# Performance work log

Measured on AMD Instinct MI355X. Metric: run time of the kernel, lower is better.

## Reference

```python
import jax, jax.numpy as jnp
import numpy as np

COUNTS = [1536, 8192, 16384, 24576, 12288, 1024, 512, 512, 256, 128, 128]
OFFS = np.concatenate([[0], np.cumsum(COUNTS)]).astype(int).tolist()
N = OFFS[-1]          # 65536 atoms total, sorted by degree
MAX_DEG = 10
BATCH = 2048          # fixed GraphGather batch size
F_IN = 75
GC = 256
DENSE = 512
N_TASKS = 12
N_CLASSES = 2
BN_EPS = 1e-3         # keras BatchNormalization default epsilon


def _graph_conv(x, deg_adjs, w0, wself, wneigh, b):
    # deepchem GraphConv: per-degree (self @ Wself + sum_neighbors @ Wneigh + b), relu
    outs = [x[OFFS[0]:OFFS[1]] @ w0 + b[0]]  # degree-0 atoms: self transform only
    for d in range(1, MAX_DEG + 1):
        self_atoms = x[OFFS[d]:OFFS[d + 1]]            # [n_d, F]
        neigh = x[deg_adjs[d - 1]].sum(axis=1)         # gather [n_d, d, F] -> sum -> [n_d, F]
        outs.append(self_atoms @ wself[d - 1] + neigh @ wneigh[d - 1] + b[d])
    return jax.nn.relu(jnp.concatenate(outs, axis=0))


def _graph_pool(x, deg_adjs):
    # deepchem GraphPool: elementwise max over {self} U neighbors, per degree
    outs = [x[OFFS[0]:OFFS[1]]]  # degree-0 atoms pass through
    for d in range(1, MAX_DEG + 1):
        self_atoms = x[OFFS[d]:OFFS[d + 1]]
        outs.append(jnp.maximum(self_atoms, x[deg_adjs[d - 1]].max(axis=1)))
    return jnp.concatenate(outs, axis=0)


def _bn(x, g, bta, m, v):
    # inference-mode BatchNormalization (training=False -> moving stats)
    return g * (x - m) * jax.lax.rsqrt(v + BN_EPS) + bta


def setup_inputs():
    key = jax.random.key(0)
    ks = iter(jax.random.split(key, 64))
    inp = {}
    inp["atom_features"] = jax.random.normal(next(ks), (N, F_IN), jnp.float32)
    inp["degree_slice"] = jnp.asarray(
        np.stack([np.array(OFFS[:-1]), np.array(COUNTS)], axis=1), jnp.int32)
    # each molecule gets exactly N/BATCH atoms so no GraphGather segment is empty
    inp["membership"] = jax.random.permutation(
        next(ks), jnp.arange(N, dtype=jnp.int32) % BATCH)
    inp["n_samples"] = BATCH
    for d in range(1, MAX_DEG + 1):
        inp["deg_adj_%d" % d] = jax.random.randint(
            next(ks), (COUNTS[d], d), 0, N, jnp.int32)

    def lin(k, fi, fo):
        return jax.random.normal(k, (fi, fo), jnp.float32) * np.float32(1.0 / np.sqrt(fi))

    for li, fi in [(1, F_IN), (2, GC)]:
        inp["gc%d_w0" % li] = lin(next(ks), fi, GC)
        inp["gc%d_wself" % li] = jnp.stack([lin(next(ks), fi, GC) for _ in range(MAX_DEG)])
        inp["gc%d_wneigh" % li] = jnp.stack([lin(next(ks), fi, GC) for _ in range(MAX_DEG)])
        inp["gc%d_b" % li] = jnp.zeros((MAX_DEG + 1, GC), jnp.float32)
    for bi, dim in [(1, GC), (2, GC), (3, DENSE)]:
        inp["bn%d_gamma" % bi] = jnp.ones((dim,), jnp.float32)
        inp["bn%d_beta" % bi] = jnp.zeros((dim,), jnp.float32)
        inp["bn%d_mean" % bi] = jnp.zeros((dim,), jnp.float32)
        inp["bn%d_var" % bi] = jnp.ones((dim,), jnp.float32)
    inp["dense_w"] = lin(next(ks), GC, DENSE)
    inp["dense_b"] = jnp.zeros((DENSE,), jnp.float32)
    inp["out_w"] = lin(next(ks), 2 * DENSE, N_TASKS * N_CLASSES)
    inp["out_b"] = jnp.zeros((N_TASKS * N_CLASSES,), jnp.float32)
    return inp


def reference(atom_features, degree_slice, membership, n_samples,
              deg_adj_1, deg_adj_2, deg_adj_3, deg_adj_4, deg_adj_5,
              deg_adj_6, deg_adj_7, deg_adj_8, deg_adj_9, deg_adj_10,
              gc1_w0, gc1_wself, gc1_wneigh, gc1_b,
              gc2_w0, gc2_wself, gc2_wneigh, gc2_b,
              bn1_gamma, bn1_beta, bn1_mean, bn1_var,
              bn2_gamma, bn2_beta, bn2_mean, bn2_var,
              bn3_gamma, bn3_beta, bn3_mean, bn3_var,
              dense_w, dense_b, out_w, out_b):
    deg_adjs = [deg_adj_1, deg_adj_2, deg_adj_3, deg_adj_4, deg_adj_5,
                deg_adj_6, deg_adj_7, deg_adj_8, deg_adj_9, deg_adj_10]
    h = _graph_conv(atom_features, deg_adjs, gc1_w0, gc1_wself, gc1_wneigh, gc1_b)
    h = _bn(h, bn1_gamma, bn1_beta, bn1_mean, bn1_var)
    h = _graph_pool(h, deg_adjs)
    h = _graph_conv(h, deg_adjs, gc2_w0, gc2_wself, gc2_wneigh, gc2_b)
    h = _bn(h, bn2_gamma, bn2_beta, bn2_mean, bn2_var)
    h = _graph_pool(h, deg_adjs)
    h = jax.nn.relu(h @ dense_w + dense_b)
    h = _bn(h, bn3_gamma, bn3_beta, bn3_mean, bn3_var)
    # GraphGather: tanh(concat(segment_sum, segment_max))
    ssum = jax.ops.segment_sum(h, membership, num_segments=BATCH)
    smax = jax.ops.segment_max(h, membership, num_segments=BATCH)
    fp = jnp.tanh(jnp.concatenate([ssum, smax], axis=1))   # [BATCH, 2*DENSE]
    logits = (fp @ out_w + out_b).reshape(BATCH, N_TASKS, N_CLASSES)[:n_samples]
    probs = jax.nn.softmax(logits, axis=-1)
    return probs, logits, fp
```

## Files before the change

kernel.cpp:

```cpp
#include <hip/hip_runtime.h>
#include <hip/hip_fp16.h>
#include <math.h>

#define NATOMS 65536

typedef _Float16 f16_t;
typedef __attribute__((ext_vector_type(8))) _Float16 half8;
typedef __attribute__((ext_vector_type(4))) float f32x4;

__constant__ int c_offs[12] = {0,1536,9728,26112,50688,62976,64000,64512,65024,65280,65408,65536};

struct Adj { const int* p[10]; };

__device__ __forceinline__ int seg_of(int row) {
    int s = 0;
#pragma unroll
    for (int i = 1; i <= 10; ++i) s += (row >= c_offs[i]) ? 1 : 0;
    return s;
}

__device__ __forceinline__ void glds16(const f16_t* g, f16_t* l) {
    __builtin_amdgcn_global_load_lds(
        (const __attribute__((address_space(1))) unsigned int*)g,
        (__attribute__((address_space(3))) unsigned int*)l,
        16, 0, 0);
}


__global__ void pack_all(const float* __restrict__ g1w0, const float* __restrict__ g1ws,
                         const float* __restrict__ g1wn,
                         const float* __restrict__ g2w0, const float* __restrict__ g2ws,
                         const float* __restrict__ g2wn,
                         const float* __restrict__ dw, const float* __restrict__ ow,
                         f16_t* __restrict__ W1p, f16_t* __restrict__ W2p,
                         f16_t* __restrict__ Wdp, f16_t* __restrict__ Wop,
                         int* __restrict__ counts) {
    int idx = blockIdx.x * 256 + threadIdx.x;
    if (idx < 2048) counts[idx] = 0;
    if (idx < 540672) {
        int j = idx & 7, lane = (idx >> 3) & 63;
        int kb = (idx >> 9) % 6;
        int rest = idx / (512 * 6);
        int ni = rest & 15, s = rest >> 4;
        int k = kb * 32 + (lane >> 4) * 8 + j;
        int n = ni * 16 + (lane & 15);
        float v = 0.f;
        if (k < 75) v = (s == 0) ? g1w0[k*256 + n] : g1ws[((s-1)*75 + k)*256 + n];
        else if (k >= 96 && k < 171 && s > 0) v = g1wn[((s-1)*75 + (k-96))*256 + n];
        W1p[idx] = (f16_t)v;
    } else if (idx < 1982464) {
        int i2 = idx - 540672;
        int j = i2 & 7, lane = (i2 >> 3) & 63;
        int kb = (i2 >> 9) & 15;
        int rest = i2 >> 13;
        int ni = rest & 15, s = rest >> 4;
        int k = kb * 32 + (lane >> 4) * 8 + j;
        int n = ni * 16 + (lane & 15);
        float v = 0.f;
        if (k < 256) v = (s == 0) ? g2w0[k*256 + n] : g2ws[((s-1)*256 + k)*256 + n];
        else if (s > 0) v = g2wn[((s-1)*256 + (k-256))*256 + n];
        W2p[i2] = (f16_t)v;
    } else if (idx < 2113536) {
        int i2 = idx - 1982464;
        int j = i2 & 7, lane = (i2 >> 3) & 63;
        int kb = (i2 >> 9) & 7;
        int ni = (i2 >> 12) & 31;
        int k = kb * 32 + (lane >> 4) * 8 + j;
        int n = ni * 16 + (lane & 15);
        Wdp[i2] = (f16_t)dw[(size_t)k*512 + n];
    } else {
        int i2 = idx - 2113536;
        int j = i2 & 7, lane = (i2 >> 3) & 63;
        int kb = (i2 >> 9) & 31;
        int ni = i2 >> 14;
        int k = kb * 32 + (lane >> 4) * 8 + j;
        int n = ni * 16 + (lane & 15);
        Wop[i2] = (n < 24) ? (f16_t)ow[k*24 + n] : (f16_t)0.f;
    }
}

__global__ void cvt_pad(const float* __restrict__ xf, f16_t* __restrict__ xq) {
    int idx = blockIdx.x * 256 + threadIdx.x;
    int r = idx / 12;
    int cc = idx - r * 12;
    int c = cc << 3;
    f16_t o[8];
#pragma unroll
    for (int e = 0; e < 8; ++e)
        o[e] = (c + e < 75) ? (f16_t)xf[(size_t)r*75 + c + e] : (f16_t)0.f;
    *(uint4*)(xq + (size_t)r*96 + c) = *(uint4*)o;
}

template<int D, bool ISMAX, int LD>
__device__ __forceinline__ void gathD(float* v, const f16_t* __restrict__ src,
                                      const int* __restrict__ ap, int c) {
    int rows[D];
#pragma unroll
    for (int j = 0; j < D; ++j) rows[j] = ap[j];
    uint4 raw[D];
#pragma unroll
    for (int j = 0; j < D; ++j) raw[j] = *(const uint4*)(src + (size_t)rows[j]*LD + c);
#pragma unroll
    for (int j = 0; j < D; ++j) {
        const f16_t* u = (const f16_t*)&raw[j];
#pragma unroll
        for (int e = 0; e < 8; ++e) {
            float f = (float)u[e];
            v[e] = ISMAX ? fmaxf(v[e], f) : (v[e] + f);
        }
    }
}

template<bool ISMAX, int LD>
__device__ __forceinline__ void gath_switch(float* v, const f16_t* __restrict__ src,
                                            const int* __restrict__ ap, int s, int c) {
    switch (s) {
        case 1:  gathD<1,ISMAX,LD>(v,src,ap,c);  break;
        case 2:  gathD<2,ISMAX,LD>(v,src,ap,c);  break;
        case 3:  gathD<3,ISMAX,LD>(v,src,ap,c);  break;
        case 4:  gathD<4,ISMAX,LD>(v,src,ap,c);  break;
        case 5:  gathD<5,ISMAX,LD>(v,src,ap,c);  break;
        case 6:  gathD<6,ISMAX,LD>(v,src,ap,c);  break;
        case 7:  gathD<7,ISMAX,LD>(v,src,ap,c);  break;
        case 8:  gathD<8,ISMAX,LD>(v,src,ap,c);  break;
        case 9:  gathD<9,ISMAX,LD>(v,src,ap,c);  break;
        case 10: gathD<10,ISMAX,LD>(v,src,ap,c); break;
        default: break;
    }
}

__global__ __launch_bounds__(256) void nbsum_x(const f16_t* __restrict__ xq,
                                               f16_t* __restrict__ NBX, Adj adj) {
    int idx = blockIdx.x * 256 + threadIdx.x;
    int r = idx >> 4;
    int cc = idx & 15;
    if (cc >= 12) return;
    int c = cc << 3;
    int s = seg_of(r);
    float v[8];
#pragma unroll
    for (int e = 0; e < 8; ++e) v[e] = 0.f;
    if (s > 0)
        gath_switch<false,96>(v, xq, adj.p[s-1] + (size_t)(r - c_offs[s]) * s, s, c);
    f16_t o[8];
#pragma unroll
    for (int e = 0; e < 8; ++e) o[e] = (f16_t)v[e];
    *(uint4*)(NBX + (size_t)(r>>4)*1536 + (c>>5)*512 + ((c>>3)&3)*128 + (r&15)*8) = *(uint4*)o;
}

template<bool BLOB>
__global__ __launch_bounds__(256) void pool_k(const f16_t* __restrict__ H,
                                              f16_t* __restrict__ P, Adj adj) {
    int idx = blockIdx.x * 256 + threadIdx.x;
    int r = idx >> 5;
    int c = (idx & 31) << 3;
    int s = seg_of(r);
    uint4 self = *(const uint4*)(H + (size_t)r*256 + c);
    const f16_t* hp = (const f16_t*)&self;
    float v[8];
#pragma unroll
    for (int e = 0; e < 8; ++e) v[e] = (float)hp[e];
    if (s > 0)
        gath_switch<true,256>(v, H, adj.p[s-1] + (size_t)(r - c_offs[s]) * s, s, c);
    f16_t o[8];
#pragma unroll
    for (int e = 0; e < 8; ++e) o[e] = (f16_t)v[e];
    if (BLOB)
        *(uint4*)(P + (size_t)(r>>4)*4096 + (c>>5)*512 + ((c>>3)&3)*128 + (r&15)*8) = *(uint4*)o;
    else
        *(uint4*)(P + (size_t)r*256 + c) = *(uint4*)o;
}

__global__ __launch_bounds__(256) void nbsum_k(const f16_t* __restrict__ P,
                                               f16_t* __restrict__ NB, Adj adj) {
    int idx = blockIdx.x * 256 + threadIdx.x;
    int r = idx >> 5;
    int c = (idx & 31) << 3;
    int s = seg_of(r);
    float v[8];
#pragma unroll
    for (int e = 0; e < 8; ++e) v[e] = 0.f;
    if (s > 0)
        gath_switch<false,256>(v, P, adj.p[s-1] + (size_t)(r - c_offs[s]) * s, s, c);
    f16_t o[8];
#pragma unroll
    for (int e = 0; e < 8; ++e) o[e] = (f16_t)v[e];
    *(uint4*)(NB + (size_t)(r>>4)*4096 + (c>>5)*512 + ((c>>3)&3)*128 + (r&15)*8) = *(uint4*)o;
}

template<int K, int KSPLIT, int LDA, int NKBA1, int N, int NY, bool SEG>
__global__ __launch_bounds__(256)
void gemm_rm(const f16_t* __restrict__ A0, const f16_t* __restrict__ A1,
             const f16_t* __restrict__ Wp,
             const float* __restrict__ bias,
             const float* __restrict__ bng, const float* __restrict__ bnb,
             const float* __restrict__ bnm, const float* __restrict__ bnv,
             f16_t* __restrict__ C)
{
    constexpr int NKB = K / 32;
    constexpr int KSPB = KSPLIT / 32;
    constexpr int NNT = N / 16;
    __shared__ char smem[32768];
    f16_t* sm = (f16_t*)smem;
    f16_t* eps = (f16_t*)smem;

    const int t = threadIdx.x;
    const int lane = t & 63, wave = t >> 6;
    const int wm = wave >> 1, wn = wave & 1;
    const int quad = lane >> 4, l16 = lane & 15;
    const int id = blockIdx.x;
    const int xcd = id & 7;
    const int jj = id >> 3;
    const int xi = jj / NY;
    const int y  = jj - xi * NY;
    const int r0 = (xi * 8 + xcd) * 128;
    const int n0 = y * 128;
    const int seg = SEG ? seg_of(r0) : 0;
    const int nbase = n0 >> 4;
    const int rtg = r0 >> 4;

    f32x4 acc[4][4];
#pragma unroll
    for (int mi = 0; mi < 4; ++mi)
#pragma unroll
        for (int ni = 0; ni < 4; ++ni) acc[mi][ni] = (f32x4){0.f,0.f,0.f,0.f};

    size_t aoff[2];
#pragma unroll
    for (int i = 0; i < 2; ++i)
        aoff[i] = (size_t)(r0 + (wave*2 + i)*16 + l16) * LDA + quad*8;
    size_t bbase[2];
#pragma unroll
    for (int i = 0; i < 2; ++i)
        bbase[i] = ((size_t)(seg*NNT + nbase + wave*2 + i) * NKB) * 512 + lane*8;

#pragma unroll
    for (int kbp = 0; kbp < NKB/2; ++kbp) {
#pragma unroll
        for (int u = 0; u < 2; ++u) {
            const int kb = kbp*2 + u;
#pragma unroll
            for (int i = 0; i < 2; ++i) {
                const int rt = wave*2 + i;
                if (kb < KSPB) {
                    glds16(A0 + (size_t)kb*32 + aoff[i], sm + u*4096 + rt*512);
                } else {
                    glds16(A1 + ((size_t)(rtg + rt)*NKBA1 + (kb - KSPB))*512 + lane*8,
                           sm + u*4096 + rt*512);
                }
                glds16(Wp + bbase[i] + (size_t)kb*512, sm + 8192 + u*4096 + rt*512);
            }
        }
        __syncthreads();
#pragma unroll
        for (int u = 0; u < 2; ++u) {
            half8 a[4], b[4];
#pragma unroll
            for (int mi = 0; mi < 4; ++mi)
                a[mi] = *(const half8*)(sm + u*4096 + (wm*4 + mi)*512 + lane*8);
#pragma unroll
            for (int ni = 0; ni < 4; ++ni)
                b[ni] = *(const half8*)(sm + 8192 + u*4096 + (wn*4 + ni)*512 + lane*8);
#pragma unroll
            for (int mi = 0; mi < 4; ++mi)
#pragma unroll
                for (int ni = 0; ni < 4; ++ni)
                    acc[mi][ni] = __builtin_amdgcn_mfma_f32_16x16x32_f16(a[mi], b[ni], acc[mi][ni], 0, 0, 0);
        }
        __syncthreads();
    }

#pragma unroll
    for (int p = 0; p < 2; ++p) {
        if (wm == p) {
#pragma unroll
            for (int ni = 0; ni < 4; ++ni) {
                const int lcol = (wn*4 + ni)*16 + l16;
                const int col = n0 + lcol;
                const float scale = bng[col] * rsqrtf(bnv[col] + 1e-3f);
                const float shift = bnb[col] - bnm[col] * scale;
                const float bv = bias[(SEG ? seg*N : 0) + col];
#pragma unroll
                for (int mi = 0; mi < 4; ++mi) {
                    const int lrowb = mi*16 + quad*4;
#pragma unroll
                    for (int r = 0; r < 4; ++r) {
                        float v = acc[mi][ni][r] + bv;
                        v = fmaxf(v, 0.f);
                        v = fmaf(v, scale, shift);
                        eps[(lrowb + r)*136 + lcol] = (f16_t)v;
                    }
                }
            }
        }
        __syncthreads();
#pragma unroll
        for (int it = 0; it < 4; ++it) {
            int row = it*16 + (t >> 4);
            int ch  = t & 15;
            uint4 v = *(const uint4*)&eps[row*136 + ch*8];
            *(uint4*)(C + (size_t)(r0 + p*64 + row)*N + n0 + ch*8) = v;
        }
        __syncthreads();
    }
}

template<int NKB, int N, int NY>
__global__ __launch_bounds__(256)
void gemm_bl(const f16_t* __restrict__ A,
             const f16_t* __restrict__ Wp,
             const float* __restrict__ bias,
             const float* __restrict__ bng, const float* __restrict__ bnb,
             const float* __restrict__ bnm, const float* __restrict__ bnv,
             f16_t* __restrict__ C)
{
    constexpr int NNT = N / 16;
    __shared__ char smem[32768];
    f16_t* sm = (f16_t*)smem;
    f16_t* eps = (f16_t*)smem;

    const int t = threadIdx.x;
    const int lane = t & 63, wave = t >> 6;
    const int wm = wave >> 1, wn = wave & 1;
    const int quad = lane >> 4, l16 = lane & 15;
    const int id = blockIdx.x;
    const int xcd = id & 7;
    const int jj = id >> 3;
    const int xi = jj / NY;
    const int y  = jj - xi * NY;
    const int r0 = (xi * 8 + xcd) * 128;
    const int n0 = y * 128;
    const int nbase = n0 >> 4;
    const int rtg = r0 >> 4;

    f32x4 acc[4][4];
#pragma unroll
    for (int mi = 0; mi < 4; ++mi)
#pragma unroll
        for (int ni = 0; ni < 4; ++ni) acc[mi][ni] = (f32x4){0.f,0.f,0.f,0.f};

#pragma unroll
    for (int kbp = 0; kbp < NKB/2; ++kbp) {
#pragma unroll
        for (int u = 0; u < 2; ++u) {
            const int kb = kbp*2 + u;
#pragma unroll
            for (int i = 0; i < 2; ++i) {
                const int rt = wave*2 + i;
                glds16(A + ((size_t)(rtg + rt)*NKB + kb)*512 + lane*8, sm + u*4096 + rt*512);
                glds16(Wp + ((size_t)(nbase + rt)*NKB + kb)*512 + lane*8,
                       sm + 8192 + u*4096 + rt*512);
            }
        }
        __syncthreads();
#pragma unroll
        for (int u = 0; u < 2; ++u) {
            half8 a[4], b[4];
#pragma unroll
            for (int mi = 0; mi < 4; ++mi)
                a[mi] = *(const half8*)(sm + u*4096 + (wm*4 + mi)*512 + lane*8);
#pragma unroll
            for (int ni = 0; ni < 4; ++ni)
                b[ni] = *(const half8*)(sm + 8192 + u*4096 + (wn*4 + ni)*512 + lane*8);
#pragma unroll
            for (int mi = 0; mi < 4; ++mi)
#pragma unroll
                for (int ni = 0; ni < 4; ++ni)
                    acc[mi][ni] = __builtin_amdgcn_mfma_f32_16x16x32_f16(a[mi], b[ni], acc[mi][ni], 0, 0, 0);
        }
        __syncthreads();
    }

#pragma unroll
    for (int p = 0; p < 2; ++p) {
        if (wm == p) {
#pragma unroll
            for (int ni = 0; ni < 4; ++ni) {
                const int lcol = (wn*4 + ni)*16 + l16;
                const int col = n0 + lcol;
                const float scale = bng[col] * rsqrtf(bnv[col] + 1e-3f);
                const float shift = bnb[col] - bnm[col] * scale;
                const float bv = bias[col];
#pragma unroll
                for (int mi = 0; mi < 4; ++mi) {
                    const int lrowb = mi*16 + quad*4;
#pragma unroll
                    for (int r = 0; r < 4; ++r) {
                        float v = acc[mi][ni][r] + bv;
                        v = fmaxf(v, 0.f);
                        v = fmaf(v, scale, shift);
                        eps[(lrowb + r)*136 + lcol] = (f16_t)v;
                    }
                }
            }
        }
        __syncthreads();
#pragma unroll
        for (int it = 0; it < 4; ++it) {
            int row = it*16 + (t >> 4);
            int ch  = t & 15;
            uint4 v = *(const uint4*)&eps[row*136 + ch*8];
            *(uint4*)(C + (size_t)(r0 + p*64 + row)*N + n0 + ch*8) = v;
        }
        __syncthreads();
    }
}

__global__ void scatter_k(const int* __restrict__ mem, int* __restrict__ counts, int* __restrict__ slots) {
    int i = blockIdx.x * 256 + threadIdx.x;
    int s = mem[i];
    int p = atomicAdd(&counts[s], 1);
    if (p < 32) slots[s*32 + p] = i;
}

__global__ __launch_bounds__(64)
void reduce_k(const f16_t* __restrict__ H3, const int* __restrict__ slots,
              float* __restrict__ fp) {
    int s = blockIdx.x, l = threadIdx.x;
    int c = l * 8;
    const int* sl = slots + s*32;
    float sm[8], mx[8];
#pragma unroll
    for (int e = 0; e < 8; ++e) { sm[e] = 0.f; mx[e] = -INFINITY; }
#pragma unroll
    for (int i = 0; i < 32; ++i) {
        int a = sl[i];
        uint4 raw = *(const uint4*)(H3 + (size_t)a*512 + c);
        const f16_t* u = (const f16_t*)&raw;
#pragma unroll
        for (int e = 0; e < 8; ++e) {
            float f = (float)u[e];
            sm[e] += f;
            mx[e] = fmaxf(mx[e], f);
        }
    }
    float o1[8], o2[8];
#pragma unroll
    for (int e = 0; e < 8; ++e) {
        o1[e] = tanhf(sm[e]); o2[e] = tanhf(mx[e]);
    }
    float* fr = fp + (size_t)s*1024;
    *(float4*)(fr + c)       = *(float4*)&o1[0];
    *(float4*)(fr + c + 4)   = *(float4*)&o1[4];
    *(float4*)(fr + 512 + c)     = *(float4*)&o2[0];
    *(float4*)(fr + 512 + c + 4) = *(float4*)&o2[4];
}

__global__ __launch_bounds__(256)
void final_mfma(const float* __restrict__ fp, const f16_t* __restrict__ Wop,
                const float* __restrict__ out_b,
                float* __restrict__ probs, float* __restrict__ logits) {
    const int t = threadIdx.x;
    const int lane = t & 63, wave = t >> 6;
    const int quad = lane >> 4, l16 = lane & 15;
    const int r0 = (blockIdx.x * 4 + wave) * 16;

    f32x4 acc[2];
#pragma unroll
    for (int ni = 0; ni < 2; ++ni) acc[ni] = (f32x4){0.f,0.f,0.f,0.f};

    const size_t rowoff = (size_t)(r0 + l16) * 1024 + quad*8;
    size_t boff[2];
#pragma unroll
    for (int ni = 0; ni < 2; ++ni)
        boff[ni] = (size_t)ni * 32 * 512 + lane*8;

    auto loadA = [&](half8& a, int kb) {
        const float* src = fp + rowoff + kb*32;
        float4 u0 = *(const float4*)(src);
        float4 u1 = *(const float4*)(src + 4);
        half8 h;
        h[0] = (f16_t)u0.x; h[1] = (f16_t)u0.y; h[2] = (f16_t)u0.z; h[3] = (f16_t)u0.w;
        h[4] = (f16_t)u1.x; h[5] = (f16_t)u1.y; h[6] = (f16_t)u1.z; h[7] = (f16_t)u1.w;
        a = h;
    };
    auto loadB = [&](half8* b, int kb) {
#pragma unroll
        for (int ni = 0; ni < 2; ++ni) b[ni] = *(const half8*)(Wop + boff[ni] + (size_t)kb*512);
    };
    auto domfma = [&](half8& a, half8* b) {
#pragma unroll
        for (int ni = 0; ni < 2; ++ni)
            acc[ni] = __builtin_amdgcn_mfma_f32_16x16x32_f16(a, b[ni], acc[ni], 0, 0, 0);
    };

    half8 a0, b0[2], a1, b1[2];
    loadA(a0, 0); loadB(b0, 0);
#pragma unroll
    for (int kb = 0; kb < 32; kb += 2) {
        loadA(a1, kb + 1); loadB(b1, kb + 1);
        domfma(a0, b0);
        if (kb + 2 < 32) { loadA(a0, kb + 2); loadB(b0, kb + 2); }
        domfma(a1, b1);
    }

#pragma unroll
    for (int ni = 0; ni < 2; ++ni) {
        const int c = ni*16 + l16;
        const bool ok = (c < 24);
        const float bv = ok ? out_b[c] : 0.f;
#pragma unroll
        for (int r = 0; r < 4; ++r) {
            float lg = acc[ni][r] + bv;
            float lp = __shfl_xor(lg, 1);
            float m = fmaxf(lg, lp);
            float e  = expf(lg - m);
            float ep = expf(lp - m);
            float pr = e / (e + ep);
            if (ok) {
                int row = r0 + quad*4 + r;
                logits[(size_t)row*24 + c] = lg;
                probs[(size_t)row*24 + c]  = pr;
            }
        }
    }
}

extern "C" void kernel_launch(void* const* d_in, const int* in_sizes, int n_in,
                              void* d_out, int out_size, void* d_ws, size_t ws_size,
                              hipStream_t stream) {
    const float* atom       = (const float*)d_in[0];
    const int*   membership = (const int*)  d_in[2];
    Adj adj;
    for (int d = 0; d < 10; ++d) adj.p[d] = (const int*)d_in[4+d];
    const float* gc1_w0     = (const float*)d_in[14];
    const float* gc1_wself  = (const float*)d_in[15];
    const float* gc1_wneigh = (const float*)d_in[16];
    const float* gc1_b      = (const float*)d_in[17];
    const float* gc2_w0     = (const float*)d_in[18];
    const float* gc2_wself  = (const float*)d_in[19];
    const float* gc2_wneigh = (const float*)d_in[20];
    const float* gc2_b      = (const float*)d_in[21];
    const float* bn1g = (const float*)d_in[22]; const float* bn1b = (const float*)d_in[23];
    const float* bn1m = (const float*)d_in[24]; const float* bn1v = (const float*)d_in[25];
    const float* bn2g = (const float*)d_in[26]; const float* bn2b = (const float*)d_in[27];
    const float* bn2m = (const float*)d_in[28]; const float* bn2v = (const float*)d_in[29];
    const float* bn3g = (const float*)d_in[30]; const float* bn3b = (const float*)d_in[31];
    const float* bn3m = (const float*)d_in[32]; const float* bn3v = (const float*)d_in[33];
    const float* dense_w = (const float*)d_in[34];
    const float* dense_b = (const float*)d_in[35];
    const float* out_w   = (const float*)d_in[36];
    const float* out_b   = (const float*)d_in[37];

    f16_t* wsb = (f16_t*)d_ws;
    f16_t* xq    = wsb;
    f16_t* NBX   = wsb + 6291456;
    f16_t* H1b   = wsb + 12582912;
    f16_t* P1rm  = wsb + 29360128;
    f16_t* NB2b  = wsb + 46137344;
    f16_t* H2b   = H1b;
    f16_t* P2bl  = NB2b;
    f16_t* H3b   = H1b;
    f16_t* W1p   = wsb + 62914560;
    f16_t* W2p   = wsb + 63455232;
    f16_t* Wdp   = wsb + 64897024;
    f16_t* Wop   = wsb + 65028096;
    int*  counts = (int*)(wsb + 65060864);
    int*  slots  = counts + 2048;

    float* outp   = (float*)d_out;
    float* probs  = outp;
    float* logits = outp + 49152;
    float* fp     = outp + 98304;

    pack_all<<<8384, 256, 0, stream>>>(gc1_w0, gc1_wself, gc1_wneigh,
                                       gc2_w0, gc2_wself, gc2_wneigh,
                                       dense_w, out_w,
                                       W1p, W2p, Wdp, Wop, counts);

    cvt_pad<<<(NATOMS*12)/256, 256, 0, stream>>>(atom, xq);
    nbsum_x<<<(NATOMS*16)/256, 256, 0, stream>>>(xq, NBX, adj);
    gemm_rm<192,96,96,3,256,2,true><<<1024, 256, 0, stream>>>(
        xq, NBX, W1p, gc1_b, bn1g, bn1b, bn1m, bn1v, H1b);
    pool_k<false><<<(NATOMS*32)/256, 256, 0, stream>>>(H1b, P1rm, adj);

    nbsum_k<<<(NATOMS*32)/256, 256, 0, stream>>>(P1rm, NB2b, adj);
    gemm_rm<512,256,256,8,256,2,true><<<1024, 256, 0, stream>>>(
        P1rm, NB2b, W2p, gc2_b, bn2g, bn2b, bn2m, bn2v, H2b);
    pool_k<true><<<(NATOMS*32)/256, 256, 0, stream>>>(H2b, P2bl, adj);

    gemm_bl<8,512,4><<<2048, 256, 0, stream>>>(
        P2bl, Wdp, dense_b, bn3g, bn3b, bn3m, bn3v, H3b);

    scatter_k<<<NATOMS/256, 256, 0, stream>>>(membership, counts, slots);
    reduce_k<<<2048, 64, 0, stream>>>(H3b, slots, fp);

    final_mfma<<<32, 256, 0, stream>>>(fp, Wop, out_b, probs, logits);
}
```

Before: 358.2 us.

## Merge small launches and split segment reduce across four waves

Folds the feature-conversion kernel into the weight-packing launch and the membership scatter into the first neighbor-sum launch, which removes two kernel launches. The segment reduction now uses four waves per molecule, each summing eight atoms, and combines their partials through shared memory. The final output GEMM is relaunched with one wave per block across more blocks. Together these aim to cut launch overhead and raise parallelism in the small tail kernels, at the cost of extra LDS traffic and a barrier in the reduction.

Result: faster. 339.8 us (-5.1%).

```diff
diff --git a/kernel.cpp b/kernel.cpp
--- a/kernel.cpp
+++ b/kernel.cpp
@@ -27,14 +27,27 @@
 }
 
 
-__global__ void pack_all(const float* __restrict__ g1w0, const float* __restrict__ g1ws,
+__global__ void pack_cvt(const float* __restrict__ g1w0, const float* __restrict__ g1ws,
                          const float* __restrict__ g1wn,
                          const float* __restrict__ g2w0, const float* __restrict__ g2ws,
                          const float* __restrict__ g2wn,
                          const float* __restrict__ dw, const float* __restrict__ ow,
                          f16_t* __restrict__ W1p, f16_t* __restrict__ W2p,
                          f16_t* __restrict__ Wdp, f16_t* __restrict__ Wop,
-                         int* __restrict__ counts) {
+                         int* __restrict__ counts,
+                         const float* __restrict__ xf, f16_t* __restrict__ xq) {
+    if (blockIdx.x >= 8384) {
+        int idx = (blockIdx.x - 8384) * 256 + threadIdx.x;
+        int r = idx / 12;
+        int cc = idx - r * 12;
+        int c = cc << 3;
+        f16_t o[8];
+#pragma unroll
+        for (int e = 0; e < 8; ++e)
+            o[e] = (c + e < 75) ? (f16_t)xf[(size_t)r*75 + c + e] : (f16_t)0.f;
+        *(uint4*)(xq + (size_t)r*96 + c) = *(uint4*)o;
+        return;
+    }
     int idx = blockIdx.x * 256 + threadIdx.x;
     if (idx < 2048) counts[idx] = 0;
     if (idx < 540672) {
@@ -79,18 +92,6 @@
     }
 }
 
-__global__ void cvt_pad(const float* __restrict__ xf, f16_t* __restrict__ xq) {
-    int idx = blockIdx.x * 256 + threadIdx.x;
-    int r = idx / 12;
-    int cc = idx - r * 12;
-    int c = cc << 3;
-    f16_t o[8];
-#pragma unroll
-    for (int e = 0; e < 8; ++e)
-        o[e] = (c + e < 75) ? (f16_t)xf[(size_t)r*75 + c + e] : (f16_t)0.f;
-    *(uint4*)(xq + (size_t)r*96 + c) = *(uint4*)o;
-}
-
 template<int D, bool ISMAX, int LD>
 __device__ __forceinline__ void gathD(float* v, const f16_t* __restrict__ src,
                                       const int* __restrict__ ap, int c) {
@@ -129,8 +130,18 @@
     }
 }
 
-__global__ __launch_bounds__(256) void nbsum_x(const f16_t* __restrict__ xq,
-                                               f16_t* __restrict__ NBX, Adj adj) {
+__global__ __launch_bounds__(256) void nbsum_sc(const f16_t* __restrict__ xq,
+                                                f16_t* __restrict__ NBX, Adj adj,
+                                                const int* __restrict__ mem,
+                                                int* __restrict__ counts,
+                                                int* __restrict__ slots) {
+    if (blockIdx.x >= 4096) {
+        int i = (blockIdx.x - 4096) * 256 + threadIdx.x;
+        int s = mem[i];
+        int p = atomicAdd(&counts[s], 1);
+        if (p < 32) slots[s*32 + p] = i;
+        return;
+    }
     int idx = blockIdx.x * 256 + threadIdx.x;
     int r = idx >> 4;
     int cc = idx & 15;
@@ -406,24 +417,21 @@
     }
 }
 
-__global__ void scatter_k(const int* __restrict__ mem, int* __restrict__ counts, int* __restrict__ slots) {
-    int i = blockIdx.x * 256 + threadIdx.x;
-    int s = mem[i];
-    int p = atomicAdd(&counts[s], 1);
-    if (p < 32) slots[s*32 + p] = i;
-}
-
-__global__ __launch_bounds__(64)
+__global__ __launch_bounds__(256)
 void reduce_k(const f16_t* __restrict__ H3, const int* __restrict__ slots,
               float* __restrict__ fp) {
-    int s = blockIdx.x, l = threadIdx.x;
+    __shared__ float shs[3][512];
+    __shared__ float shm[3][512];
+    int s = blockIdx.x;
+    int t = threadIdx.x;
+    int w = t >> 6, l = t & 63;
     int c = l * 8;
-    const int* sl = slots + s*32;
+    const int* sl = slots + s*32 + w*8;
     float sm[8], mx[8];
 #pragma unroll
     for (int e = 0; e < 8; ++e) { sm[e] = 0.f; mx[e] = -INFINITY; }
 #pragma unroll
-    for (int i = 0; i < 32; ++i) {
+    for (int i = 0; i < 8; ++i) {
         int a = sl[i];
         uint4 raw = *(const uint4*)(H3 + (size_t)a*512 + c);
         const f16_t* u = (const f16_t*)&raw;
@@ -434,26 +442,42 @@
             mx[e] = fmaxf(mx[e], f);
         }
     }
-    float o1[8], o2[8];
-#pragma unroll
-    for (int e = 0; e < 8; ++e) {
-        o1[e] = tanhf(sm[e]); o2[e] = tanhf(mx[e]);
-    }
-    float* fr = fp + (size_t)s*1024;
-    *(float4*)(fr + c)       = *(float4*)&o1[0];
-    *(float4*)(fr + c + 4)   = *(float4*)&o1[4];
-    *(float4*)(fr + 512 + c)     = *(float4*)&o2[0];
-    *(float4*)(fr + 512 + c + 4) = *(float4*)&o2[4];
-}
-
-__global__ __launch_bounds__(256)
+    if (w) {
+        *(float4*)&shs[w-1][c]   = *(float4*)&sm[0];
+        *(float4*)&shs[w-1][c+4] = *(float4*)&sm[4];
+        *(float4*)&shm[w-1][c]   = *(float4*)&mx[0];
+        *(float4*)&shm[w-1][c+4] = *(float4*)&mx[4];
+    }
+    __syncthreads();
+    if (w == 0) {
+#pragma unroll
+        for (int j = 0; j < 3; ++j)
+#pragma unroll
+            for (int e = 0; e < 8; ++e) {
+                sm[e] += shs[j][c+e];
+                mx[e] = fmaxf(mx[e], shm[j][c+e]);
+            }
+        float o1[8], o2[8];
+#pragma unroll
+        for (int e = 0; e < 8; ++e) {
+            o1[e] = tanhf(sm[e]); o2[e] = tanhf(mx[e]);
+        }
+        float* fr = fp + (size_t)s*1024;
+        *(float4*)(fr + c)       = *(float4*)&o1[0];
+        *(float4*)(fr + c + 4)   = *(float4*)&o1[4];
+        *(float4*)(fr + 512 + c)     = *(float4*)&o2[0];
+        *(float4*)(fr + 512 + c + 4) = *(float4*)&o2[4];
+    }
+}
+
+__global__ __launch_bounds__(64)
 void final_mfma(const float* __restrict__ fp, const f16_t* __restrict__ Wop,
                 const float* __restrict__ out_b,
                 float* __restrict__ probs, float* __restrict__ logits) {
     const int t = threadIdx.x;
-    const int lane = t & 63, wave = t >> 6;
+    const int lane = t & 63;
     const int quad = lane >> 4, l16 = lane & 15;
-    const int r0 = (blockIdx.x * 4 + wave) * 16;
+    const int r0 = blockIdx.x * 16;
 
     f32x4 acc[2];
 #pragma unroll
@@ -563,13 +587,13 @@
     float* logits = outp + 49152;
     float* fp     = outp + 98304;
 
-    pack_all<<<8384, 256, 0, stream>>>(gc1_w0, gc1_wself, gc1_wneigh,
-                                       gc2_w0, gc2_wself, gc2_wneigh,
-                                       dense_w, out_w,
-                                       W1p, W2p, Wdp, Wop, counts);
-
-    cvt_pad<<<(NATOMS*12)/256, 256, 0, stream>>>(atom, xq);
-    nbsum_x<<<(NATOMS*16)/256, 256, 0, stream>>>(xq, NBX, adj);
+    pack_cvt<<<11456, 256, 0, stream>>>(gc1_w0, gc1_wself, gc1_wneigh,
+                                        gc2_w0, gc2_wself, gc2_wneigh,
+                                        dense_w, out_w,
+                                        W1p, W2p, Wdp, Wop, counts,
+                                        atom, xq);
+
+    nbsum_sc<<<4352, 256, 0, stream>>>(xq, NBX, adj, membership, counts, slots);
     gemm_rm<192,96,96,3,256,2,true><<<1024, 256, 0, stream>>>(
         xq, NBX, W1p, gc1_b, bn1g, bn1b, bn1m, bn1v, H1b);
     pool_k<false><<<(NATOMS*32)/256, 256, 0, stream>>>(H1b, P1rm, adj);
@@ -582,8 +606,7 @@
     gemm_bl<8,512,4><<<2048, 256, 0, stream>>>(
         P2bl, Wdp, dense_b, bn3g, bn3b, bn3m, bn3v, H3b);
 
-    scatter_k<<<NATOMS/256, 256, 0, stream>>>(membership, counts, slots);
-    reduce_k<<<2048, 64, 0, stream>>>(H3b, slots, fp);
-
-    final_mfma<<<32, 256, 0, stream>>>(fp, Wop, out_b, probs, logits);
-}
+    reduce_k<<<2048, 256, 0, stream>>>(H3b, slots, fp);
+
+    final_mfma<<<128, 64, 0, stream>>>(fp, Wop, out_b, probs, logits);
+}
```
